# Optimization experiments

Measured on AMD Instinct MI355X. Metric: run time of the kernel, lower is better.

The kernel has to match this reference:

```python
import jax, jax.numpy as jnp
import numpy as np

K = 9   # kernel_size (neighbors)
D = 1   # dilation


def setup_inputs() -> dict:
    key = jax.random.key(0)
    k1, k2 = jax.random.split(key)
    B, C, N, OUT = 8, 64, 4096, 128
    x = jax.random.normal(k1, (B, C, N), dtype=jnp.float32)
    W = jax.random.normal(k2, (OUT, 2 * C), dtype=jnp.float32) * 0.05
    b = jnp.zeros((OUT,), dtype=jnp.float32)
    return {"x": x, "W": W, "b": b}


def dilated_knn(x, k, d):
    # x: [B, C, N] -> nn_idx: [B, N, k] (indices of k nearest neighbors, dilated)
    x = jax.lax.stop_gradient(x)  # original detaches x for graph construction
    x2 = jnp.sum(x * x, axis=1)                      # [B, N]
    inner = jnp.einsum('bcn,bcm->bnm', x, x)         # [B, N, N]
    neg_dist = 2.0 * inner - x2[:, :, None] - x2[:, None, :]  # -||xi-xj||^2
    _, idx = jax.lax.top_k(neg_dist, k * d)          # [B, N, k*d]
    return idx[..., ::d]                             # dilated selection -> [B, N, k]


def reference(x, W, b):
    # x: [B, C, N]
    nn_idx = dilated_knn(x, K, D)                    # [B, N, k]
    # gather neighbor features: x_j[b, c, n, kk] = x[b, c, nn_idx[b, n, kk]]
    x_j = jax.vmap(lambda xb, ib: xb[:, ib])(x, nn_idx)  # [B, C, N, k]
    # max-relative: max_k (x_j - x_i)
    x_max = jnp.max(x_j - x[:, :, :, None], axis=-1)     # [B, C, N]
    h = jnp.concatenate([x, x_max], axis=1)              # [B, 2C, N]
    # 1x1 conv + bias + ReLU
    out = jnp.einsum('oc,bcn->bon', W, h) + b[None, :, None]
    return jax.nn.relu(out)
```

## Files before the change

kernel.cpp:

```cpp
#include <hip/hip_runtime.h>
#include <float.h>

#define B_   8
#define C_   64
#define N_   4096
#define OUT_ 128
#define KNN  9
#define CAP  64
#define TAU_A 2.15f

typedef __attribute__((ext_vector_type(8))) short short8;
typedef __attribute__((ext_vector_type(4))) float f32x4;

__device__ inline unsigned short f2bf(float f) {
    unsigned u = __float_as_uint(f);
    unsigned r = (u + 0x7fffu + ((u >> 16) & 1u)) >> 16;
    return (unsigned short)r;
}
__device__ inline float bf2f(unsigned short s) {
    return __uint_as_float(((unsigned)s) << 16);
}


__global__ void k_transpose(const float* __restrict__ x, float* __restrict__ xT,
                            float* __restrict__ x2, unsigned short* __restrict__ xfrag,
                            const float* __restrict__ W, unsigned short* __restrict__ wfrag) {
    __shared__ float t[C_][65];
    int tid = threadIdx.x;
    if (blockIdx.x >= 512) {
        int mt = blockIdx.x - 512;
        int kc = tid >> 6, L = tid & 63;
        int o  = mt * 16 + (L & 15);
        int c0 = kc * 32 + ((L >> 4) * 8);
        const float* src = W + (size_t)o * 128 + c0;
        float4 v0 = *(const float4*)src, v1 = *(const float4*)(src + 4);
        float vs[8] = {v0.x, v0.y, v0.z, v0.w, v1.x, v1.y, v1.z, v1.w};
        short8 hi, lo;
#pragma unroll
        for (int j = 0; j < 8; ++j) {
            unsigned short hb = f2bf(vs[j]);
            float hf = bf2f(hb);
            lo[j] = (short)f2bf(vs[j] - hf);
            hi[j] = (short)hb;
        }
        size_t cb = (size_t)(mt * 4 + kc) * 2 * 512;
        *(short8*)(wfrag + cb + L * 8)       = hi;
        *(short8*)(wfrag + cb + 512 + L * 8) = lo;
        return;
    }
    int b  = blockIdx.x & 7;
    int n0 = (blockIdx.x >> 3) * 64;
    for (int i = 0; i < 4; ++i) {
        int f = i * 256 + tid;
        int c = f >> 4, n4 = f & 15;
        float4 v = *(const float4*)(x + ((size_t)b * C_ + c) * N_ + n0 + n4 * 4);
        t[c][n4 * 4 + 0] = v.x;
        t[c][n4 * 4 + 1] = v.y;
        t[c][n4 * 4 + 2] = v.z;
        t[c][n4 * 4 + 3] = v.w;
    }
    __syncthreads();
    for (int i = 0; i < 4; ++i) {
        int f = i * 256 + tid;
        int n = f >> 4, c4 = f & 15;
        float4 v = {t[c4 * 4 + 0][n], t[c4 * 4 + 1][n],
                    t[c4 * 4 + 2][n], t[c4 * 4 + 3][n]};
        *(float4*)(xT + ((size_t)b * N_ + n0 + n) * C_ + c4 * 4) = v;
    }
    int q = tid >> 6, L = tid & 63;
    int mloc = q * 16 + (L & 15);
    int k8 = (L >> 4) * 8;
    size_t cb = (size_t)(b * 256 + (n0 >> 4) + q) * 2 * 512;
#pragma unroll
    for (int h = 0; h < 2; ++h) {
        short8 hi;
#pragma unroll
        for (int j = 0; j < 8; ++j)
            hi[j] = (short)f2bf(t[h * 32 + k8 + j][mloc]);
        *(short8*)(xfrag + cb + h * 512 + L * 8) = hi;
    }
    if (tid < 64) {
        float s = 0.f;
        for (int c = 0; c < C_; ++c) { float v = t[c][tid]; s += v * v; }
        x2[(size_t)b * N_ + n0 + tid] = s;
    }
}

#define APPEND(KEY, TAU, LN, MIDX)                                      \
    if ((KEY) > (TAU)) {                                                \
        unsigned u = __float_as_uint(KEY);                              \
        u = (u & 0x80000000u) ? ~u : (u | 0x80000000u);                 \
        unsigned pk = (u & 0xFFFFF000u) | (unsigned)(MIDX);             \
        int sl = atomicAdd(&cnt_s[LN], 1);                              \
        if (sl < CAP) buf_s[LN][sl] = pk;                               \
    }

__global__ __launch_bounds__(512, 4) void k_topk_mf(const unsigned short* __restrict__ xfrag,
                                                    const float* __restrict__ x2,
                                                    unsigned* __restrict__ cand24,
                                                    int* __restrict__ cnt2) {
    __shared__ int cnt_s[64];
    __shared__ unsigned buf_s[64][CAP];
    int b    = blockIdx.x & 7;
    int mh   = (blockIdx.x >> 3) & 1;
    int ng   = blockIdx.x >> 4;
    int wave = threadIdx.x >> 6, lane = threadIdx.x & 63;
    if (threadIdx.x < 64) cnt_s[threadIdx.x] = 0;

    const short8* fr = (const short8*)xfrag;

    short8 Bh[4][2];
#pragma unroll
    for (int q = 0; q < 4; ++q)
#pragma unroll
        for (int h = 0; h < 2; ++h) {
            int ch = ((b * 256 + ng * 4 + q) * 2 + h);
            Bh[q][h] = fr[(size_t)ch * 64 + lane];
        }

    float tau[4];
#pragma unroll
    for (int q = 0; q < 4; ++q) {
        float x2n = x2[b * N_ + ng * 64 + q * 16 + (lane & 15)];
        tau[q] = TAU_A * sqrtf(fmaf(4.f, x2n, 128.f)) - 64.f;
    }

    int mt0 = mh * 128 + wave * 16;
    const short8* pA = fr + (size_t)(b * 256 + mt0) * 2 * 64 + lane;
    const f32x4*  px2 = (const f32x4*)(x2 + b * N_ + mt0 * 16 + (lane >> 4) * 4);
    short8 Ah0 = pA[0], Ah1 = pA[64];
    f32x4 x2v = *px2;

    __syncthreads();

    for (int i = 0; i < 16; ++i) {
        if (i != 15) { pA += 128; px2 += 4; }
        short8 nAh0 = pA[0], nAh1 = pA[64];
        f32x4 nx2 = *px2;

        int mbase = (mt0 + i) * 16 + (lane >> 4) * 4;

#pragma unroll
        for (int q = 0; q < 4; ++q) {
            f32x4 acc = {0.f, 0.f, 0.f, 0.f};
            acc = __builtin_amdgcn_mfma_f32_16x16x32_bf16(Ah0, Bh[q][0], acc, 0, 0, 0);
            acc = __builtin_amdgcn_mfma_f32_16x16x32_bf16(Ah1, Bh[q][1], acc, 0, 0, 0);
            float k0 = fmaf(2.f, acc[0], -x2v[0]);
            float k1 = fmaf(2.f, acc[1], -x2v[1]);
            float k2 = fmaf(2.f, acc[2], -x2v[2]);
            float k3 = fmaf(2.f, acc[3], -x2v[3]);
            float kmax = fmaxf(fmaxf(k0, k1), fmaxf(k2, k3));
            if (kmax > tau[q]) {
                int ln = q * 16 + (lane & 15);
                APPEND(k0, tau[q], ln, mbase + 0)
                APPEND(k1, tau[q], ln, mbase + 1)
                APPEND(k2, tau[q], ln, mbase + 2)
                APPEND(k3, tau[q], ln, mbase + 3)
            }
        }
        Ah0 = nAh0; Ah1 = nAh1; x2v = nx2;
    }

    __syncthreads();
    if (threadIdx.x < 64) {
        int r = threadIdx.x;
        int c = cnt_s[r];
        size_t grow = (size_t)b * N_ + ng * 64 + r;
        cnt2[grow * 2 + mh] = c;
        int cc = min(c, CAP);
        unsigned best[12];
#pragma unroll
        for (int j = 0; j < 12; ++j) best[j] = 0u;
        for (int s = 0; s < cc; ++s) {
            unsigned v = buf_s[r][s];
            if (v > best[0]) {
                best[0] = v;
#pragma unroll
                for (int j = 0; j < 11; ++j) {
                    bool sw = best[j] > best[j + 1];
                    unsigned t = best[j];
                    best[j]     = sw ? best[j + 1] : best[j];
                    best[j + 1] = sw ? t : best[j + 1];
                }
            }
        }
#pragma unroll
        for (int j = 0; j < 12; ++j)
            cand24[grow * 24 + mh * 12 + j] = best[11 - j];
    }
}

__global__ __launch_bounds__(256) void k_refine(const float* __restrict__ xT,
                                                const unsigned* __restrict__ cand24,
                                                const int* __restrict__ cnt2,
                                                int* __restrict__ idx9) {
    __shared__ double kk[4][2][24];
    __shared__ int    ki[4][2][24];
    int wave = threadIdx.x >> 6, lane = threadIdx.x & 63;
    int half = lane >> 5, hl = lane & 31;
    int b = blockIdx.x & 7;
    int row = b * N_ + (blockIdx.x >> 3) * 8 + wave * 2 + half;
    int c0 = cnt2[(size_t)row * 2 + 0];
    int c1 = cnt2[(size_t)row * 2 + 1];
    bool ok = (c0 + c1 >= KNN) && (c0 <= CAP) && (c1 <= CAP);
    int c0c = min(c0, 12), c1c = min(c1, 12);

    double mykey = -1e300; int myidx = 0x7fffffff;
    bool valid = ok && (hl < 24) && ((hl < 12) ? (hl < c0c) : ((hl - 12) < c1c));
    if (valid) {
        int m = (int)(cand24[(size_t)row * 24 + hl] & 0xFFFu);
        const float* xi = xT + (size_t)row * C_;
        const float* xm = xT + (((size_t)b << 12) + m) * C_;
        double d0 = 0.0, d1 = 0.0, s0 = 0.0, s1 = 0.0;
#pragma unroll
        for (int c4 = 0; c4 < 16; c4 += 2) {
            float4 a0 = *(const float4*)(xi + c4 * 4);
            float4 a1 = *(const float4*)(xi + c4 * 4 + 4);
            float4 v0 = *(const float4*)(xm + c4 * 4);
            float4 v1 = *(const float4*)(xm + c4 * 4 + 4);
            d0 = fma((double)a0.x, (double)v0.x, d0);  s0 = fma((double)v0.x, (double)v0.x, s0);
            d0 = fma((double)a0.y, (double)v0.y, d0);  s0 = fma((double)v0.y, (double)v0.y, s0);
            d0 = fma((double)a0.z, (double)v0.z, d0);  s0 = fma((double)v0.z, (double)v0.z, s0);
            d0 = fma((double)a0.w, (double)v0.w, d0);  s0 = fma((double)v0.w, (double)v0.w, s0);
            d1 = fma((double)a1.x, (double)v1.x, d1);  s1 = fma((double)v1.x, (double)v1.x, s1);
            d1 = fma((double)a1.y, (double)v1.y, d1);  s1 = fma((double)v1.y, (double)v1.y, s1);
            d1 = fma((double)a1.z, (double)v1.z, d1);  s1 = fma((double)v1.z, (double)v1.z, s1);
            d1 = fma((double)a1.w, (double)v1.w, d1);  s1 = fma((double)v1.w, (double)v1.w, s1);
        }
        mykey = 2.0 * (d0 + d1) - (s0 + s1);
        myidx = m;
    }
    if (hl < 24) { kk[wave][half][hl] = mykey; ki[wave][half][hl] = myidx; }
    if (valid) {
        int r = 0;
#pragma unroll
        for (int k = 0; k < 24; ++k) {
            double ok2 = kk[wave][half][k]; int oi = ki[wave][half][k];
            r += (ok2 > mykey || (ok2 == mykey && oi < myidx)) ? 1 : 0;
        }
        if (r < KNN) idx9[(size_t)row * KNN + r] = myidx;
    }
}

__global__ void k_fallback(const float* __restrict__ xT, const int* __restrict__ cnt2,
                           int* __restrict__ idx9) {
    int wave = threadIdx.x >> 6, lane = threadIdx.x & 63;
    int row = blockIdx.x * 4 + wave;
    int c0 = cnt2[(size_t)row * 2 + 0];
    int c1 = cnt2[(size_t)row * 2 + 1];
    if ((c0 + c1 >= KNN) && (c0 <= CAP) && (c1 <= CAP)) return;
    int b = row >> 12;
    const float* xi = xT + (size_t)row * C_;
    float4 xr[16];
#pragma unroll
    for (int c4 = 0; c4 < 16; ++c4) xr[c4] = *(const float4*)(xi + c4 * 4);
    double sk[9]; int si[9];
#pragma unroll
    for (int j = 0; j < 9; ++j) { sk[j] = -1e300; si[j] = 0x7fffffff; }
    for (int mb = 0; mb < N_; mb += 64) {
        int m = mb + lane;
        const float* xm = xT + (((size_t)b << 12) + m) * C_;
        double d0 = 0.0, d1 = 0.0, s0 = 0.0, s1 = 0.0;
#pragma unroll
        for (int c4 = 0; c4 < 16; c4 += 2) {
            float4 v = *(const float4*)(xm + c4 * 4);
            float4 w = *(const float4*)(xm + c4 * 4 + 4);
            float4 a = xr[c4], bb = xr[c4 + 1];
            d0 = fma((double)a.x, (double)v.x, d0);  s0 = fma((double)v.x, (double)v.x, s0);
            d0 = fma((double)a.y, (double)v.y, d0);  s0 = fma((double)v.y, (double)v.y, s0);
            d0 = fma((double)a.z, (double)v.z, d0);  s0 = fma((double)v.z, (double)v.z, s0);
            d0 = fma((double)a.w, (double)v.w, d0);  s0 = fma((double)v.w, (double)v.w, s0);
            d1 = fma((double)bb.x, (double)w.x, d1); s1 = fma((double)w.x, (double)w.x, s1);
            d1 = fma((double)bb.y, (double)w.y, d1); s1 = fma((double)w.y, (double)w.y, s1);
            d1 = fma((double)bb.z, (double)w.z, d1); s1 = fma((double)w.z, (double)w.z, s1);
            d1 = fma((double)bb.w, (double)w.w, d1); s1 = fma((double)w.w, (double)w.w, s1);
        }
        double key = 2.0 * (d0 + d1) - (s0 + s1);
        if (key > sk[0] || (key == sk[0] && m < si[0])) {
            sk[0] = key; si[0] = m;
#pragma unroll
            for (int j = 0; j < 8; ++j) {
                bool sw = (sk[j] > sk[j + 1]) || (sk[j] == sk[j + 1] && si[j] < si[j + 1]);
                double tk = sk[j]; int ti = si[j];
                sk[j]     = sw ? sk[j + 1] : sk[j];
                si[j]     = sw ? si[j + 1] : si[j];
                sk[j + 1] = sw ? tk : sk[j + 1];
                si[j + 1] = sw ? ti : si[j + 1];
            }
        }
    }
    for (int r = 0; r < KNN; ++r) {
        double k = sk[8]; int ix = si[8];
#pragma unroll
        for (int o = 32; o; o >>= 1) {
            double ok = __shfl_xor(k, o); int oi = __shfl_xor(ix, o);
            bool take = (ok > k) || (ok == k && oi < ix);
            k = take ? ok : k; ix = take ? oi : ix;
        }
        if (lane == 0) idx9[(size_t)row * KNN + r] = ix;
        if (si[8] == ix) {
#pragma unroll
            for (int j = 8; j > 0; --j) { sk[j] = sk[j - 1]; si[j] = si[j - 1]; }
            sk[0] = -1e300; si[0] = 0x7fffffff;
        }
    }
}

__global__ __launch_bounds__(256, 2) void k_gemm(const float* __restrict__ xT,
                                                 const int* __restrict__ idx9,
                                                 const unsigned short* __restrict__ wfrag,
                                                 const float* __restrict__ bias,
                                                 float* __restrict__ out) {
    __shared__ float h[128][65];
    int b  = blockIdx.x & 7;
    int n0 = (blockIdx.x >> 3) * 64;
    int wave = threadIdx.x >> 6, lane = threadIdx.x & 63;

    const short8* fw = (const short8*)wfrag;
    short8 Wh[2][4], Wl[2][4];
#pragma unroll
    for (int t = 0; t < 2; ++t)
#pragma unroll
        for (int kc = 0; kc < 4; ++kc) {
            size_t cb = (size_t)((wave * 2 + t) * 4 + kc) * 2 * 64;
            Wh[t][kc] = fw[cb + lane];
            Wl[t][kc] = fw[cb + 64 + lane];
        }

    for (int r = 0; r < 16; ++r) {
        int nn = wave * 16 + r;
        size_t row = (size_t)b * N_ + n0 + nn;
        const int* id = idx9 + row * KNN;
        float m = -FLT_MAX;
#pragma unroll
        for (int k = 0; k < KNN; ++k) {
            int j = id[k];
            m = fmaxf(m, xT[(((size_t)b << 12) + j) * C_ + lane]);
        }
        float xic = xT[row * C_ + lane];
        h[lane][nn]      = xic;
        h[64 + lane][nn] = m - xic;
    }
    __syncthreads();

    f32x4 acc[2][4];
#pragma unroll
    for (int t = 0; t < 2; ++t)
#pragma unroll
        for (int nt = 0; nt < 4; ++nt) acc[t][nt] = (f32x4){0.f, 0.f, 0.f, 0.f};

    int cb0 = (lane >> 4) * 8;
    int nl  = lane & 15;
#pragma unroll
    for (int kc = 0; kc < 4; ++kc) {
#pragma unroll
        for (int nt = 0; nt < 4; ++nt) {
            short8 bh, bl;
#pragma unroll
            for (int j = 0; j < 8; ++j) {
                float v = h[kc * 32 + cb0 + j][nt * 16 + nl];
                unsigned short hb = f2bf(v);
                bl[j] = (short)f2bf(v - bf2f(hb));
                bh[j] = (short)hb;
            }
#pragma unroll
            for (int t = 0; t < 2; ++t) {
                acc[t][nt] = __builtin_amdgcn_mfma_f32_16x16x32_bf16(Wh[t][kc], bh, acc[t][nt], 0, 0, 0);
                acc[t][nt] = __builtin_amdgcn_mfma_f32_16x16x32_bf16(Wl[t][kc], bh, acc[t][nt], 0, 0, 0);
                acc[t][nt] = __builtin_amdgcn_mfma_f32_16x16x32_bf16(Wh[t][kc], bl, acc[t][nt], 0, 0, 0);
            }
        }
    }
    __syncthreads();

    f32x4 bs[2];
#pragma unroll
    for (int t = 0; t < 2; ++t)
        bs[t] = *(const f32x4*)(bias + wave * 32 + t * 16 + (lane >> 4) * 4);
#pragma unroll
    for (int t = 0; t < 2; ++t)
#pragma unroll
        for (int nt = 0; nt < 4; ++nt)
#pragma unroll
            for (int j = 0; j < 4; ++j) {
                float v = acc[t][nt][j] + bs[t][j];
                h[wave * 32 + t * 16 + (lane >> 4) * 4 + j][nt * 16 + nl] = fmaxf(v, 0.f);
            }
    __syncthreads();

#pragma unroll
    for (int rr = 0; rr < 32; ++rr) {
        int o = wave * 32 + rr;
        out[((size_t)b * OUT_ + o) * N_ + n0 + lane] = h[o][lane];
    }
}

extern "C" void kernel_launch(void* const* d_in, const int* in_sizes, int n_in,
                              void* d_out, int out_size, void* d_ws, size_t ws_size,
                              hipStream_t stream) {
    const float* x    = (const float*)d_in[0];
    const float* W    = (const float*)d_in[1];
    const float* bias = (const float*)d_in[2];
    float* out = (float*)d_out;
    char* ws = (char*)d_ws;

    float*          xT     = (float*)(ws);
    unsigned short* xfrag  = (unsigned short*)(ws + 8388608);
    int*            idx9   = (int*)(ws + 8388608);
    float*          x2     = (float*)(ws + 16777216);
    unsigned short* wfrag  = (unsigned short*)(ws + 16908288);
    unsigned*       cand24 = (unsigned*)(ws + 16973824);
    int*            cnt2   = (int*)(ws + 20119552);

    k_transpose<<<dim3(520),  dim3(256), 0, stream>>>(x, xT, x2, xfrag, W, wfrag);
    k_topk_mf  <<<dim3(1024), dim3(512), 0, stream>>>(xfrag, x2, cand24, cnt2);
    k_refine   <<<dim3(4096), dim3(256), 0, stream>>>(xT, cand24, cnt2, idx9);
    k_fallback <<<dim3(8192), dim3(256), 0, stream>>>(xT, cnt2, idx9);
    k_gemm     <<<dim3(512),  dim3(256), 0, stream>>>(xT, idx9, wfrag, bias, out);
}
```

Measured before the change: 112.9 us.

## Split KNN candidate search into four column quarters with smaller blocks

```diff
diff --git a/kernel.cpp b/kernel.cpp
--- a/kernel.cpp
+++ b/kernel.cpp
@@ -95,15 +95,15 @@
         if (sl < CAP) buf_s[LN][sl] = pk;                               \
     }
 
-__global__ __launch_bounds__(512, 4) void k_topk_mf(const unsigned short* __restrict__ xfrag,
+__global__ __launch_bounds__(256, 4) void k_topk_mf(const unsigned short* __restrict__ xfrag,
                                                     const float* __restrict__ x2,
-                                                    unsigned* __restrict__ cand24,
-                                                    int* __restrict__ cnt2) {
+                                                    unsigned* __restrict__ cand48,
+                                                    int* __restrict__ cnt4) {
     __shared__ int cnt_s[64];
     __shared__ unsigned buf_s[64][CAP];
     int b    = blockIdx.x & 7;
-    int mh   = (blockIdx.x >> 3) & 1;
-    int ng   = blockIdx.x >> 4;
+    int mq   = (blockIdx.x >> 3) & 3;
+    int ng   = blockIdx.x >> 5;
     int wave = threadIdx.x >> 6, lane = threadIdx.x & 63;
     if (threadIdx.x < 64) cnt_s[threadIdx.x] = 0;
 
@@ -125,7 +125,7 @@
         tau[q] = TAU_A * sqrtf(fmaf(4.f, x2n, 128.f)) - 64.f;
     }
 
-    int mt0 = mh * 128 + wave * 16;
+    int mt0 = mq * 64 + wave * 16;
     const short8* pA = fr + (size_t)(b * 256 + mt0) * 2 * 64 + lane;
     const f32x4*  px2 = (const f32x4*)(x2 + b * N_ + mt0 * 16 + (lane >> 4) * 4);
     short8 Ah0 = pA[0], Ah1 = pA[64];
@@ -166,7 +166,7 @@
         int r = threadIdx.x;
         int c = cnt_s[r];
         size_t grow = (size_t)b * N_ + ng * 64 + r;
-        cnt2[grow * 2 + mh] = c;
+        cnt4[grow * 4 + mq] = c;
         int cc = min(c, CAP);
         unsigned best[12];
 #pragma unroll
@@ -186,29 +186,32 @@
         }
 #pragma unroll
         for (int j = 0; j < 12; ++j)
-            cand24[grow * 24 + mh * 12 + j] = best[11 - j];
+            cand48[grow * 48 + mq * 12 + j] = best[11 - j];
     }
 }
 
 __global__ __launch_bounds__(256) void k_refine(const float* __restrict__ xT,
-                                                const unsigned* __restrict__ cand24,
-                                                const int* __restrict__ cnt2,
+                                                const unsigned* __restrict__ cand48,
+                                                const int* __restrict__ cnt4,
                                                 int* __restrict__ idx9) {
-    __shared__ double kk[4][2][24];
-    __shared__ int    ki[4][2][24];
+    __shared__ double kk[4][48];
+    __shared__ int    ki[4][48];
     int wave = threadIdx.x >> 6, lane = threadIdx.x & 63;
-    int half = lane >> 5, hl = lane & 31;
     int b = blockIdx.x & 7;
-    int row = b * N_ + (blockIdx.x >> 3) * 8 + wave * 2 + half;
-    int c0 = cnt2[(size_t)row * 2 + 0];
-    int c1 = cnt2[(size_t)row * 2 + 1];
-    bool ok = (c0 + c1 >= KNN) && (c0 <= CAP) && (c1 <= CAP);
-    int c0c = min(c0, 12), c1c = min(c1, 12);
+    int row = b * N_ + (blockIdx.x >> 3) * 4 + wave;
+    int c0 = cnt4[(size_t)row * 4 + 0];
+    int c1 = cnt4[(size_t)row * 4 + 1];
+    int c2 = cnt4[(size_t)row * 4 + 2];
+    int c3 = cnt4[(size_t)row * 4 + 3];
+    int cmax = max(max(c0, c1), max(c2, c3));
+    bool ok = (c0 + c1 + c2 + c3 >= KNN) && (cmax <= CAP);
+    int qq = lane / 12, slot = lane - qq * 12;
+    int cq = (qq == 0) ? c0 : (qq == 1) ? c1 : (qq == 2) ? c2 : c3;
 
     double mykey = -1e300; int myidx = 0x7fffffff;
-    bool valid = ok && (hl < 24) && ((hl < 12) ? (hl < c0c) : ((hl - 12) < c1c));
+    bool valid = ok && (lane < 48) && (slot < min(cq, 12));
     if (valid) {
-        int m = (int)(cand24[(size_t)row * 24 + hl] & 0xFFFu);
+        int m = (int)(cand48[(size_t)row * 48 + lane] & 0xFFFu);
         const float* xi = xT + (size_t)row * C_;
         const float* xm = xT + (((size_t)b << 12) + m) * C_;
         double d0 = 0.0, d1 = 0.0, s0 = 0.0, s1 = 0.0;
@@ -230,25 +233,28 @@
         mykey = 2.0 * (d0 + d1) - (s0 + s1);
         myidx = m;
     }
-    if (hl < 24) { kk[wave][half][hl] = mykey; ki[wave][half][hl] = myidx; }
+    if (lane < 48) { kk[wave][lane] = mykey; ki[wave][lane] = myidx; }
     if (valid) {
         int r = 0;
 #pragma unroll
-        for (int k = 0; k < 24; ++k) {
-            double ok2 = kk[wave][half][k]; int oi = ki[wave][half][k];
+        for (int k = 0; k < 48; ++k) {
+            double ok2 = kk[wave][k]; int oi = ki[wave][k];
             r += (ok2 > mykey || (ok2 == mykey && oi < myidx)) ? 1 : 0;
         }
         if (r < KNN) idx9[(size_t)row * KNN + r] = myidx;
     }
 }
 
-__global__ void k_fallback(const float* __restrict__ xT, const int* __restrict__ cnt2,
+__global__ void k_fallback(const float* __restrict__ xT, const int* __restrict__ cnt4,
                            int* __restrict__ idx9) {
     int wave = threadIdx.x >> 6, lane = threadIdx.x & 63;
     int row = blockIdx.x * 4 + wave;
-    int c0 = cnt2[(size_t)row * 2 + 0];
-    int c1 = cnt2[(size_t)row * 2 + 1];
-    if ((c0 + c1 >= KNN) && (c0 <= CAP) && (c1 <= CAP)) return;
+    int c0 = cnt4[(size_t)row * 4 + 0];
+    int c1 = cnt4[(size_t)row * 4 + 1];
+    int c2 = cnt4[(size_t)row * 4 + 2];
+    int c3 = cnt4[(size_t)row * 4 + 3];
+    int cmax = max(max(c0, c1), max(c2, c3));
+    if ((c0 + c1 + c2 + c3 >= KNN) && (cmax <= CAP)) return;
     int b = row >> 12;
     const float* xi = xT + (size_t)row * C_;
     float4 xr[16];
@@ -409,12 +415,12 @@
     int*            idx9   = (int*)(ws + 8388608);
     float*          x2     = (float*)(ws + 16777216);
     unsigned short* wfrag  = (unsigned short*)(ws + 16908288);
-    unsigned*       cand24 = (unsigned*)(ws + 16973824);
-    int*            cnt2   = (int*)(ws + 20119552);
+    unsigned*       cand48 = (unsigned*)(ws + 16973824);
+    int*            cnt4   = (int*)(ws + 23265280);
 
     k_transpose<<<dim3(520),  dim3(256), 0, stream>>>(x, xT, x2, xfrag, W, wfrag);
-    k_topk_mf  <<<dim3(1024), dim3(512), 0, stream>>>(xfrag, x2, cand24, cnt2);
-    k_refine   <<<dim3(4096), dim3(256), 0, stream>>>(xT, cand24, cnt2, idx9);
-    k_fallback <<<dim3(8192), dim3(256), 0, stream>>>(xT, cnt2, idx9);
+    k_topk_mf  <<<dim3(2048), dim3(256), 0, stream>>>(xfrag, x2, cand48, cnt4);
+    k_refine   <<<dim3(8192), dim3(256), 0, stream>>>(xT, cand48, cnt4, idx9);
+    k_fallback <<<dim3(8192), dim3(256), 0, stream>>>(xT, cnt4, idx9);
     k_gemm     <<<dim3(512),  dim3(256), 0, stream>>>(xT, idx9, wfrag, bias, out);
 }
```

Result: slower. 135.4 us (+19.9%).
